# Optimization experiments

Hardware: AMD Instinct MI355X
Metric: run time of the kernel (lower is better)

## Reference

```python
import jax, jax.numpy as jnp
import numpy as np

B, T, D, H, C = 128, 1000, 40, 128, 8  # batch, time, input feats, hidden, classes


def _lstm_layer(x, Wih, Whh, bih, bhh):
    """Unidirectional LSTM over time. x: [B,T,Din] -> [B,T,H]. PyTorch gate order i,f,g,o."""
    Bn = x.shape[0]
    Hn = Whh.shape[1]
    b = bih + bhh
    def step(carry, xt):
        h, c = carry
        g = xt @ Wih.T + h @ Whh.T + b  # [B,4H]
        i, f, gg, o = jnp.split(g, 4, axis=-1)
        c = jax.nn.sigmoid(f) * c + jax.nn.sigmoid(i) * jnp.tanh(gg)
        h = jax.nn.sigmoid(o) * jnp.tanh(c)
        return (h, c), h
    h0 = jnp.zeros((Bn, Hn), x.dtype)
    _, hs = jax.lax.scan(step, (h0, h0), jnp.swapaxes(x, 0, 1))  # scan over time
    return jnp.swapaxes(hs, 0, 1)


def _bilstm_layer(x, pf, pb):
    fwd = _lstm_layer(x, *pf)
    bwd = jnp.flip(_lstm_layer(jnp.flip(x, 1), *pb), 1)
    return jnp.concatenate([fwd, bwd], axis=-1)  # [B,T,2H]


def setup_inputs() -> dict:
    key = jax.random.key(0)
    ks = jax.random.split(key, 16)
    s = 0.05
    def rn(k, shape):
        return jax.random.normal(k, shape, jnp.float32) * s
    inp = {"x": jax.random.normal(ks[0], (B, T, D), jnp.float32)}
    inp["ln_g"] = jnp.ones((D,), jnp.float32)
    inp["ln_b"] = jnp.zeros((D,), jnp.float32)
    dims = [D, 2 * H]  # layer-0 input feats, layer-1 input feats
    i = 1
    for l in range(2):
        for d in ("f", "b"):
            inp[f"Wih_{d}{l}"] = rn(ks[i], (4 * H, dims[l])); i += 1
            inp[f"Whh_{d}{l}"] = rn(ks[i], (4 * H, H)); i += 1
            inp[f"bih_{d}{l}"] = jnp.zeros((4 * H,), jnp.float32)
            inp[f"bhh_{d}{l}"] = jnp.zeros((4 * H,), jnp.float32)
    inp["attn_W1"] = rn(ks[i], (H, 2 * H)); i += 1
    inp["attn_b1"] = jnp.zeros((H,), jnp.float32)
    inp["attn_w2"] = rn(ks[i], (1, H)); i += 1
    inp["fc_W1"] = rn(ks[i], (H, 2 * H)); i += 1
    inp["fc_b1"] = jnp.zeros((H,), jnp.float32)
    inp["fc_W2"] = rn(ks[i], (C, H)); i += 1
    inp["fc_b2"] = jnp.zeros((C,), jnp.float32)
    return inp


def reference(x, ln_g, ln_b,
              Wih_f0, Whh_f0, bih_f0, bhh_f0, Wih_b0, Whh_b0, bih_b0, bhh_b0,
              Wih_f1, Whh_f1, bih_f1, bhh_f1, Wih_b1, Whh_b1, bih_b1, bhh_b1,
              attn_W1, attn_b1, attn_w2, fc_W1, fc_b1, fc_W2, fc_b2):
    # LayerNorm over feature dim (eps=1e-5, PyTorch default)
    mu = jnp.mean(x, axis=-1, keepdims=True)
    var = jnp.var(x, axis=-1, keepdims=True)
    xn = (x - mu) * jax.lax.rsqrt(var + 1e-5) * ln_g + ln_b
    # 2-layer bidirectional LSTM
    h = _bilstm_layer(xn, (Wih_f0, Whh_f0, bih_f0, bhh_f0), (Wih_b0, Whh_b0, bih_b0, bhh_b0))
    h = _bilstm_layer(h, (Wih_f1, Whh_f1, bih_f1, bhh_f1), (Wih_b1, Whh_b1, bih_b1, bhh_b1))
    # attention pooling: Linear-Tanh-Linear(no bias) -> softmax over time
    scores = jnp.tanh(h @ attn_W1.T + attn_b1) @ attn_w2[0]  # [B,T]
    w = jax.nn.softmax(scores, axis=1)
    ctx = jnp.einsum('bt,btd->bd', w, h)  # [B,2H]
    # MLP classifier head
    hid = jax.nn.relu(ctx @ fc_W1.T + fc_b1)
    return hid @ fc_W2.T + fc_b2  # [B,C] logits
```

## Files before the change

kernel.cpp:

```cpp
#include <hip/hip_runtime.h>

#define T_ 1000

typedef float v2f __attribute__((ext_vector_type(2)));

__device__ __forceinline__ float sigf(float x) { return 1.0f / (1.0f + __expf(-x)); }
__device__ __forceinline__ float tanh_fast(float x) { return 1.0f - 2.0f / (1.0f + __expf(2.0f * x)); }
__device__ __forceinline__ float dot4(float4 a, float4 b) {
  return a.x * b.x + a.y * b.y + a.z * b.z + a.w * b.w;
}
__device__ __forceinline__ void pkfma(v2f& acc, float4 w, float4 v) {
  v2f wl; wl[0] = w.x; wl[1] = w.y;
  v2f wh; wh[0] = w.z; wh[1] = w.w;
  v2f vl; vl[0] = v.x; vl[1] = v.y;
  v2f vh; vh[0] = v.z; vh[1] = v.w;
  acc += wl * vl;
  acc += wh * vh;
}
__device__ __forceinline__ unsigned short f2bf(float f) {
  unsigned u = __float_as_uint(f);
  u = (u + 0x7fffu + ((u >> 16) & 1u)) >> 16;
  return (unsigned short)u;
}
__device__ __forceinline__ float bf2f(unsigned short h) {
  return __uint_as_float(((unsigned)h) << 16);
}
__device__ __forceinline__ float4 bf4_to_f4(ushort4 u) {
  float4 r;
  r.x = bf2f(u.x); r.y = bf2f(u.y); r.z = bf2f(u.z); r.w = bf2f(u.w);
  return r;
}

__global__ void bail_kernel(float* out, int n) {
  for (int i = threadIdx.x; i < n; i += 256) out[i] = 0.0f;
}

__global__ __launch_bounds__(256) void ln_stats_kernel(const float* __restrict__ x,
                                                       float* __restrict__ mu_arr,
                                                       float* __restrict__ rs_arr) {
  const int lane = threadIdx.x & 63;
  const int w = threadIdx.x >> 6;
  const long row = (long)blockIdx.x * 4 + w;
  float v = (lane < 40) ? x[row * 40 + lane] : 0.0f;
  float s1 = v, s2 = v * v;
  for (int m = 32; m; m >>= 1) {
    s1 += __shfl_xor(s1, m, 64);
    s2 += __shfl_xor(s2, m, 64);
  }
  if (lane == 0) {
    const float mu = s1 * (1.0f / 40.0f);
    const float var = s2 * (1.0f / 40.0f) - mu * mu;
    mu_arr[row] = mu;
    rs_arr[row] = rsqrtf(var + 1e-5f);
  }
}

__global__ __launch_bounds__(512) __attribute__((amdgpu_waves_per_eu(2, 2))) void rec0_kernel(
    const float* __restrict__ x,
    const float* __restrict__ mu_arr, const float* __restrict__ rs_arr,
    const float* __restrict__ ln_g, const float* __restrict__ ln_b,
    const float* __restrict__ Wih_f, const float* __restrict__ Whh_f,
    const float* __restrict__ bih_f, const float* __restrict__ bhh_f,
    const float* __restrict__ Wih_b, const float* __restrict__ Whh_b,
    const float* __restrict__ bih_b, const float* __restrict__ bhh_b,
    float* __restrict__ h0) {
  const int tid = threadIdx.x;
  const int u = (tid >> 6) * 16 + ((tid & 63) >> 2);
  const int p = tid & 3;
  const int brow = blockIdx.x & 127;
  const int dir = blockIdx.x >> 7;
  const float* __restrict__ Wih = dir ? Wih_b : Wih_f;
  const float* __restrict__ Whh = dir ? Whh_b : Whh_f;
  const float* __restrict__ bih = dir ? bih_b : bih_f;
  const float* __restrict__ bhh = dir ? bhh_b : bhh_f;

  float4 wh[4][8];
  float4 wi[4][3];
  float S1[4], bias[4];
#pragma unroll
  for (int g = 0; g < 4; ++g) {
    const int row = g * 128 + u;
    const float4* wr = (const float4*)(Whh + row * 128 + p * 32);
#pragma unroll
    for (int ff = 0; ff < 8; ++ff) wh[g][ff] = wr[(ff + 2 * p) & 7];
    float s1p = 0.0f, s2p = 0.0f;
#pragma unroll
    for (int f = 0; f < 3; ++f) {
      float tmp[4];
#pragma unroll
      for (int e = 0; e < 4; ++e) {
        const int k = p * 12 + f * 4 + e;
        const float wv = (k < 40) ? Wih[row * 40 + k] : 0.0f;
        const float gk = (k < 40) ? ln_g[k] : 0.0f;
        const float bk = (k < 40) ? ln_b[k] : 0.0f;
        const float wf = wv * gk;
        tmp[e] = wf;
        s1p += wf;
        s2p += wv * bk;
      }
      wi[g][f] = make_float4(tmp[0], tmp[1], tmp[2], tmp[3]);
    }
    s1p += __shfl_xor(s1p, 1, 64); s1p += __shfl_xor(s1p, 2, 64);
    s2p += __shfl_xor(s2p, 1, 64); s2p += __shfl_xor(s2p, 2, 64);
    S1[g] = s1p;
    bias[g] = bih[g * 128 + u] + bhh[g * 128 + u] + s2p;
  }

  __shared__ float h4f[2][128];
  __shared__ __align__(16) float x_ring[2][8][48];
  __shared__ float mu_ring[2][8], rs_ring[2][8];
  __shared__ float hring[2][8][128];

  const int lr8 = tid / 40;
  const int lcol = tid - lr8 * 40;
  const long xbase = (long)brow * T_ * 40;
  const long mbase = (long)brow * T_;
  const long hbase = (long)brow * T_ * 256;

  if (tid < 128) h4f[0][tid] = 0.0f;
  if (tid < 128) {
    const int b = tid >> 6, r = (tid >> 3) & 7, cc = 40 + (tid & 7);
    x_ring[b][r][cc] = 0.0f;
  }
  if (tid < 320) {
    const int t = lr8;
    const int tt = dir ? (T_ - 1 - t) : t;
    x_ring[0][lr8][lcol] = x[xbase + (long)tt * 40 + lcol];
  } else if (tid < 328) {
    const int t = tid - 320;
    const int tt = dir ? (T_ - 1 - t) : t;
    mu_ring[0][t] = mu_arr[mbase + tt];
  } else if (tid < 336) {
    const int t = tid - 328;
    const int tt = dir ? (T_ - 1 - t) : t;
    rs_ring[0][t] = rs_arr[mbase + tt];
  }
  float c = 0.0f;
  float xpf = 0.0f, mupf = 0.0f, rspf = 0.0f;
  __syncthreads();

  for (int sb = 0; sb < 125; ++sb) {
    const int rb = sb & 1;
#pragma unroll
    for (int su = 0; su < 8; ++su) {
      const int rdq = su & 1, wrq = rdq ^ 1;
      if (su == 0) {
        if (sb + 1 < 125) {
          if (tid < 320) {
            const int t = (sb + 1) * 8 + lr8;
            const int tt = dir ? (T_ - 1 - t) : t;
            xpf = x[xbase + (long)tt * 40 + lcol];
          } else if (tid < 328) {
            const int t = (sb + 1) * 8 + (tid - 320);
            const int tt = dir ? (T_ - 1 - t) : t;
            mupf = mu_arr[mbase + tt];
          } else if (tid < 336) {
            const int t = (sb + 1) * 8 + (tid - 328);
            const int tt = dir ? (T_ - 1 - t) : t;
            rspf = rs_arr[mbase + tt];
          }
        }
        if (sb > 0) {
#pragma unroll
          for (int e = 0; e < 2; ++e) {
            const int idx = tid + e * 512;
            const int v = idx >> 7, j = idx & 127;
            const int ts = (sb - 1) * 8 + v;
            const int te = dir ? (T_ - 1 - ts) : ts;
            h0[hbase + (long)te * 256 + dir * 128 + j] = hring[rb ^ 1][v][j];
          }
        }
      }
      v2f hacc[4], xacc[4];
#pragma unroll
      for (int g = 0; g < 4; ++g) { hacc[g] = 0.0f; xacc[g] = 0.0f; }
      const float4* h4v = (const float4*)h4f[rdq];
#pragma unroll
      for (int ff = 0; ff < 8; ++ff) {
        const float4 hv = h4v[p * 8 + ((ff + 2 * p) & 7)];
        pkfma(hacc[0], wh[0][ff], hv);
        pkfma(hacc[1], wh[1][ff], hv);
        pkfma(hacc[2], wh[2][ff], hv);
        pkfma(hacc[3], wh[3][ff], hv);
      }
      const float4* xr4 = (const float4*)x_ring[rb][su];
#pragma unroll
      for (int f = 0; f < 3; ++f) {
        const float4 xv = xr4[p * 3 + f];
        pkfma(xacc[0], wi[0][f], xv);
        pkfma(xacc[1], wi[1][f], xv);
        pkfma(xacc[2], wi[2][f], xv);
        pkfma(xacc[3], wi[3][f], xv);
      }
      const float rs = rs_ring[rb][su];
      const float mu = mu_ring[rb][su];
      float pg[4];
#pragma unroll
      for (int g = 0; g < 4; ++g) {
        pg[g] = (hacc[g][0] + hacc[g][1]) + rs * (xacc[g][0] + xacc[g][1]);
        pg[g] += __shfl_xor(pg[g], 1, 64);
        pg[g] += __shfl_xor(pg[g], 2, 64);
        pg[g] += bias[g] - rs * mu * S1[g];
      }
      const float ig = sigf(pg[0]);
      const float fg = sigf(pg[1]);
      const float gg = tanh_fast(pg[2]);
      const float og = sigf(pg[3]);
      c = fg * c + ig * gg;
      const float hv = og * tanh_fast(c);
      if (p == 0) { h4f[wrq][u] = hv; hring[rb][su][u] = hv; }
      if (su == 7 && sb + 1 < 125) {
        if (tid < 320) x_ring[rb ^ 1][lr8][lcol] = xpf;
        else if (tid < 328) mu_ring[rb ^ 1][tid - 320] = mupf;
        else if (tid < 336) rs_ring[rb ^ 1][tid - 328] = rspf;
      }
      __syncthreads();
    }
  }
#pragma unroll
  for (int e = 0; e < 2; ++e) {
    const int idx = tid + e * 512;
    const int v = idx >> 7, j = idx & 127;
    const int ts = 124 * 8 + v;
    const int te = dir ? (T_ - 1 - ts) : ts;
    h0[hbase + (long)te * 256 + dir * 128 + j] = hring[0][v][j];
  }
}

__global__ __launch_bounds__(512) __attribute__((amdgpu_waves_per_eu(2, 2))) void rec1_kernel(
    const float* __restrict__ xw_f, const float* __restrict__ xw_b,
    const float* __restrict__ Whh_f, const float* __restrict__ bih_f, const float* __restrict__ bhh_f,
    const float* __restrict__ Whh_b, const float* __restrict__ bih_b, const float* __restrict__ bhh_b,
    unsigned short* __restrict__ h1b, float* __restrict__ state,
    int Tc, int t0f, int t0b, int first) {
  const int tid = threadIdx.x;
  const int u = (tid >> 6) * 16 + ((tid & 63) >> 2);
  const int p = tid & 3;
  const int brow = blockIdx.x & 127;
  const int dir = blockIdx.x >> 7;
  const float* __restrict__ xw = dir ? xw_b : xw_f;
  const float* __restrict__ Whh = dir ? Whh_b : Whh_f;
  const float* __restrict__ bih = dir ? bih_b : bih_f;
  const float* __restrict__ bhh = dir ? bhh_b : bhh_f;
  const int t0 = dir ? t0b : t0f;

  float4 wh[4][8];
#pragma unroll
  for (int g = 0; g < 4; ++g) {
    const float4* wr = (const float4*)(Whh + (g * 128 + u) * 128 + p * 32);
#pragma unroll
    for (int ff = 0; ff < 8; ++ff) wh[g][ff] = wr[(ff + 2 * p) & 7];
  }
  const int myrow = p * 128 + u;
  const float bias_p = bih[myrow] + bhh[myrow];

  __shared__ float h4f[2][128];
  __shared__ float hring[2][8][128];
  float* sblk = state + (long)blockIdx.x * 256;
  float c = 0.0f;
  if (first) {
    if (tid < 128) h4f[0][tid] = 0.0f;
  } else {
    if (tid < 128) h4f[0][tid] = sblk[tid];
    c = sblk[128 + u];
  }
  const long gbase = (long)brow * Tc;
  float xr[8];
#pragma unroll
  for (int v = 0; v < 8; ++v) {
    xr[v] = 0.0f;
    if (v < Tc) {
      const int tr = dir ? (Tc - 1 - v) : v;
      xr[v] = xw[(gbase + tr) * 512 + myrow];
    }
  }
  __syncthreads();

  const int nSB = (Tc + 7) / 8;
  for (int sb = 0; sb < nSB; ++sb) {
    const int rb = sb & 1;
#pragma unroll
    for (int su = 0; su < 8; ++su) {
      const int s = sb * 8 + su;
      if (s >= Tc) break;
      const int rdq = su & 1, wrq = rdq ^ 1;
      if (su == 0 && sb > 0) {
#pragma unroll
        for (int e = 0; e < 2; ++e) {
          const int idx = tid + e * 512;
          const int v = idx >> 7, j = idx & 127;
          const int s2 = (sb - 1) * 8 + v;
          const int tt = dir ? (Tc - 1 - s2) : s2;
          h1b[((long)brow * T_ + (t0 + tt)) * 256 + dir * 128 + j] = f2bf(hring[rb ^ 1][v][j]);
        }
      }
      v2f hacc[4];
#pragma unroll
      for (int g = 0; g < 4; ++g) hacc[g] = 0.0f;
      const float4* h4v = (const float4*)h4f[rdq];
#pragma unroll
      for (int ff = 0; ff < 8; ++ff) {
        const float4 hv = h4v[p * 8 + ((ff + 2 * p) & 7)];
        pkfma(hacc[0], wh[0][ff], hv);
        pkfma(hacc[1], wh[1][ff], hv);
        pkfma(hacc[2], wh[2][ff], hv);
        pkfma(hacc[3], wh[3][ff], hv);
      }
      const float xin = xr[su] + bias_p;
      float pg[4];
#pragma unroll
      for (int g = 0; g < 4; ++g) {
        pg[g] = hacc[g][0] + hacc[g][1] + ((p == g) ? xin : 0.0f);
        pg[g] += __shfl_xor(pg[g], 1, 64);
        pg[g] += __shfl_xor(pg[g], 2, 64);
      }
      const float ig = sigf(pg[0]);
      const float fg = sigf(pg[1]);
      const float gg = tanh_fast(pg[2]);
      const float og = sigf(pg[3]);
      c = fg * c + ig * gg;
      const float hv = og * tanh_fast(c);
      if (p == 0) { h4f[wrq][u] = hv; hring[rb][su][u] = hv; }
      if (su == 7) {
#pragma unroll
        for (int v = 0; v < 8; ++v) {
          const int sn = s + 1 + v;
          xr[v] = 0.0f;
          if (sn < Tc) {
            const int tr = dir ? (Tc - 1 - sn) : sn;
            xr[v] = xw[(gbase + tr) * 512 + myrow];
          }
        }
      }
      __syncthreads();
    }
  }
  {
    const int sbL = (Tc - 1) >> 3;
    const int cnt = Tc - sbL * 8;
    const int rbL = sbL & 1;
#pragma unroll
    for (int e = 0; e < 2; ++e) {
      const int idx = tid + e * 512;
      const int v = idx >> 7, j = idx & 127;
      if (v < cnt) {
        const int s2 = sbL * 8 + v;
        const int tt = dir ? (Tc - 1 - s2) : s2;
        h1b[((long)brow * T_ + (t0 + tt)) * 256 + dir * 128 + j] = f2bf(hring[rbL][v][j]);
      }
    }
  }
  if (tid < 128) sblk[tid] = h4f[Tc & 1][tid];
  if (p == 0) sblk[128 + u] = c;
}

__global__ __launch_bounds__(256, 2) void gemm_xw1(
    const float* __restrict__ h0,
    const float* __restrict__ Wf, const float* __restrict__ Wb,
    float* __restrict__ xwf, float* __restrict__ xwb,
    int Tc, int t0f, int t0b) {
  __shared__ float As[64 * 36];
  __shared__ float Bs[128 * 36];
  __shared__ int rowbase[64];
  const int tid = threadIdx.x;
  const int tx = tid & 15, ty = tid >> 4;
  const int r0 = blockIdx.x * 64;
  const int jt = blockIdx.y;
  const int dir = jt >> 2;
  const int nh = jt & 3;
  const float* __restrict__ W = dir ? Wb : Wf;
  float* __restrict__ out = dir ? xwb : xwf;
  const int jbase = nh * 128;
  const int t0 = dir ? t0b : t0f;

  if (tid < 64) {
    const int r = r0 + tid;
    const int br = r / Tc;
    rowbase[tid] = br * T_ + t0 + (r - br * Tc);
  }

  float4* As4 = (float4*)As;
  float4* Bs4 = (float4*)Bs;
  float acc[4][8] = {};
#pragma unroll 1
  for (int kk = 0; kk < 8; ++kk) {
    __syncthreads();
#pragma unroll
    for (int i = 0; i < 2; ++i) {
      const int q = tid + i * 256;
      const int row = q >> 3, k4 = q & 7;
      As4[row * 9 + k4] = *(const float4*)&h0[(long)rowbase[row] * 256 + kk * 32 + k4 * 4];
    }
#pragma unroll
    for (int i = 0; i < 4; ++i) {
      const int q = tid + i * 256;
      const int row = q >> 3, k4 = q & 7;
      Bs4[row * 9 + k4] = *(const float4*)&W[(long)(jbase + row) * 256 + kk * 32 + k4 * 4];
    }
    __syncthreads();
#pragma unroll 1
    for (int k4 = 0; k4 < 8; ++k4) {
      float4 av[4];
#pragma unroll
      for (int r = 0; r < 4; ++r) av[r] = As4[(ty * 4 + r) * 9 + k4];
#pragma unroll
      for (int c2 = 0; c2 < 8; ++c2) {
        const float4 bv = Bs4[(tx + 16 * c2) * 9 + k4];
#pragma unroll
        for (int r = 0; r < 4; ++r) acc[r][c2] += dot4(av[r], bv);
      }
    }
  }
#pragma unroll
  for (int r = 0; r < 4; ++r) {
    const long ob = (long)(r0 + ty * 4 + r) * 512 + jbase + tx;
#pragma unroll
    for (int c2 = 0; c2 < 8; ++c2) out[ob + c2 * 16] = acc[r][c2];
  }
}

__global__ __launch_bounds__(256, 2) void score_kernel(
    const unsigned short* __restrict__ h1b, const float* __restrict__ W1,
    const float* __restrict__ b1, const float* __restrict__ w2,
    float* __restrict__ scores) {
  __shared__ float As[64 * 36];
  __shared__ float Bs[128 * 36];
  const int tid = threadIdx.x;
  const int tx = tid & 15, ty = tid >> 4;
  const long r0 = (long)blockIdx.x * 64;

  float4* As4 = (float4*)As;
  float4* Bs4 = (float4*)Bs;
  float acc[4][8] = {};
#pragma unroll 1
  for (int kk = 0; kk < 8; ++kk) {
    __syncthreads();
#pragma unroll
    for (int i = 0; i < 2; ++i) {
      const int q = tid + i * 256;
      const int row = q >> 3, k4 = q & 7;
      const ushort4 uv = *(const ushort4*)&h1b[(r0 + row) * 256 + kk * 32 + k4 * 4];
      As4[row * 9 + k4] = bf4_to_f4(uv);
    }
#pragma unroll
    for (int i = 0; i < 4; ++i) {
      const int q = tid + i * 256;
      const int row = q >> 3, k4 = q & 7;
      Bs4[row * 9 + k4] = *(const float4*)&W1[(long)row * 256 + kk * 32 + k4 * 4];
    }
    __syncthreads();
#pragma unroll 1
    for (int k4 = 0; k4 < 8; ++k4) {
      float4 av[4];
#pragma unroll
      for (int r = 0; r < 4; ++r) av[r] = As4[(ty * 4 + r) * 9 + k4];
#pragma unroll
      for (int c2 = 0; c2 < 8; ++c2) {
        const float4 bv = Bs4[(tx + 16 * c2) * 9 + k4];
#pragma unroll
        for (int r = 0; r < 4; ++r) acc[r][c2] += dot4(av[r], bv);
      }
    }
  }
#pragma unroll
  for (int r = 0; r < 4; ++r) {
    float s = 0.0f;
#pragma unroll
    for (int c2 = 0; c2 < 8; ++c2) {
      const int col = tx + 16 * c2;
      s += tanh_fast(acc[r][c2] + b1[col]) * w2[col];
    }
#pragma unroll
    for (int m = 1; m < 16; m <<= 1) s += __shfl_xor(s, m, 16);
    if (tx == 0) scores[r0 + ty * 4 + r] = s;
  }
}

__global__ __launch_bounds__(256, 2) void head_kernel(
    const float* __restrict__ scores, const unsigned short* __restrict__ h1b,
    const float* __restrict__ fW1, const float* __restrict__ fb1,
    const float* __restrict__ fW2, const float* __restrict__ fb2,
    float* __restrict__ outp) {
  const int b = blockIdx.x, tid = threadIdx.x;
  __shared__ float wls[1000];
  __shared__ float red[8];
  __shared__ __align__(16) float ctx[256];
  __shared__ __align__(16) float hid[128];

  float sv[4];
  float mx = -1e30f;
#pragma unroll
  for (int i = 0; i < 4; ++i) {
    const int t = tid + i * 256;
    sv[i] = (t < 1000) ? scores[b * 1000 + t] : -1e30f;
    mx = fmaxf(mx, sv[i]);
  }
  for (int m = 32; m; m >>= 1) mx = fmaxf(mx, __shfl_xor(mx, m, 64));
  if ((tid & 63) == 0) red[tid >> 6] = mx;
  __syncthreads();
  mx = fmaxf(fmaxf(red[0], red[1]), fmaxf(red[2], red[3]));
  float se = 0.0f;
#pragma unroll
  for (int i = 0; i < 4; ++i) {
    const int t = tid + i * 256;
    if (t < 1000) {
      const float e = __expf(sv[i] - mx);
      wls[t] = e;
      se += e;
    }
  }
  for (int m = 32; m; m >>= 1) se += __shfl_xor(se, m, 64);
  if ((tid & 63) == 0) red[4 + (tid >> 6)] = se;
  __syncthreads();
  const float rinv = 1.0f / (red[4] + red[5] + red[6] + red[7]);

  float a = 0.0f;
  const unsigned short* hb = h1b + (long)b * T_ * 256 + tid;
  for (int t = 0; t < T_; ++t) a = fmaf(wls[t], bf2f(hb[t * 256]), a);
  ctx[tid] = a * rinv;
  __syncthreads();
  if (tid < 128) {
    float s = fb1[tid];
    const float4* wr = (const float4*)&fW1[tid * 256];
    const float4* cc = (const float4*)ctx;
#pragma unroll
    for (int f = 0; f < 64; ++f) s += dot4(wr[f], cc[f]);
    hid[tid] = fmaxf(s, 0.0f);
  }
  __syncthreads();
  if (tid < 8) {
    float s = fb2[tid];
    const float4* wr = (const float4*)&fW2[tid * 128];
    const float4* hh = (const float4*)hid;
#pragma unroll
    for (int f = 0; f < 32; ++f) s += dot4(wr[f], hh[f]);
    outp[b * 8 + tid] = s;
  }
}

extern "C" void kernel_launch(void* const* d_in, const int* in_sizes, int n_in,
                              void* d_out, int out_size, void* d_ws, size_t ws_size,
                              hipStream_t stream) {
  (void)in_sizes; (void)n_in; (void)out_size;
  const float* x       = (const float*)d_in[0];
  const float* ln_g    = (const float*)d_in[1];
  const float* ln_b    = (const float*)d_in[2];
  const float* Wih_f0  = (const float*)d_in[3];
  const float* Whh_f0  = (const float*)d_in[4];
  const float* bih_f0  = (const float*)d_in[5];
  const float* bhh_f0  = (const float*)d_in[6];
  const float* Wih_b0  = (const float*)d_in[7];
  const float* Whh_b0  = (const float*)d_in[8];
  const float* bih_b0  = (const float*)d_in[9];
  const float* bhh_b0  = (const float*)d_in[10];
  const float* Wih_f1  = (const float*)d_in[11];
  const float* Whh_f1  = (const float*)d_in[12];
  const float* bih_f1  = (const float*)d_in[13];
  const float* bhh_f1  = (const float*)d_in[14];
  const float* Wih_b1  = (const float*)d_in[15];
  const float* Whh_b1  = (const float*)d_in[16];
  const float* bih_b1  = (const float*)d_in[17];
  const float* bhh_b1  = (const float*)d_in[18];
  const float* attn_W1 = (const float*)d_in[19];
  const float* attn_b1 = (const float*)d_in[20];
  const float* attn_w2 = (const float*)d_in[21];
  const float* fc_W1   = (const float*)d_in[22];
  const float* fc_b1   = (const float*)d_in[23];
  const float* fc_W2   = (const float*)d_in[24];
  const float* fc_b2   = (const float*)d_in[25];

  char* base = (char*)d_ws;
  size_t off = 0;
  auto alloc = [&](size_t bytes) {
    char* ptr = base + off;
    off += (bytes + 255) & ~(size_t)255;
    return ptr;
  };
  float*          h0    = (float*)alloc(32768000ull * 4);
  unsigned short* h1b   = (unsigned short*)alloc(32768000ull * 2);
  float*          state = (float*)alloc(65536ull * 4);
  float*          scor  = (float*)alloc(128000ull * 4);
  float*          mu_a  = (float*)alloc(128000ull * 4);
  float*          rs_a  = (float*)alloc(128000ull * 4);

  const size_t rem = (ws_size > off) ? (ws_size - off) : 0;
  static const int cands[16] = {1000, 500, 250, 200, 125, 100, 50, 40, 25, 20, 10, 8, 5, 4, 2, 1};
  int Tc = 0;
  for (int ci = 0; ci < 16; ++ci) {
    if (524288ull * (size_t)cands[ci] <= rem) { Tc = cands[ci]; break; }
  }
  if (Tc == 0) {
    bail_kernel<<<dim3(1), dim3(256), 0, stream>>>((float*)d_out, 1024);
    return;
  }
  float* xwf = (float*)(base + off);
  float* xwb = xwf + 65536L * Tc;

  ln_stats_kernel<<<dim3(32000), dim3(256), 0, stream>>>(x, mu_a, rs_a);
  rec0_kernel<<<dim3(256), dim3(512), 0, stream>>>(x, mu_a, rs_a, ln_g, ln_b,
                                                   Wih_f0, Whh_f0, bih_f0, bhh_f0,
                                                   Wih_b0, Whh_b0, bih_b0, bhh_b0, h0);
  const int nch = T_ / Tc;
  for (int ch = 0; ch < nch; ++ch) {
    const int t0f = ch * Tc;
    const int t0b = T_ - (ch + 1) * Tc;
    gemm_xw1<<<dim3(2 * Tc, 8), dim3(256), 0, stream>>>(h0, Wih_f1, Wih_b1, xwf, xwb, Tc, t0f, t0b);
    rec1_kernel<<<dim3(256), dim3(512), 0, stream>>>(xwf, xwb, Whh_f1, bih_f1, bhh_f1,
                                                     Whh_b1, bih_b1, bhh_b1, h1b, state,
                                                     Tc, t0f, t0b, (ch == 0) ? 1 : 0);
  }
  score_kernel<<<dim3(2000), dim3(256), 0, stream>>>(h1b, attn_W1, attn_b1, attn_w2, scor);
  head_kernel<<<dim3(128), dim3(256), 0, stream>>>(scor, h1b, fc_W1, fc_b1, fc_W2, fc_b2,
                                                   (float*)d_out);
}
```

Before: 3.173 ms.

## Hoist layer-0 input projection to GEMM and share fp16-LDS recurrence kernel

Layer 0 no longer fuses the LayerNorm input projection into its recurrent loop. A new chunked GEMM computes normalized x times Wih first, and both layers then use one recurrence kernel. In that kernel, half the Whh gate rows (f and o) move from registers into LDS as fp16 with an XOR swizzle, and the i and g rows stay in fp32 registers, which cuts register pressure. The GEMMs switch to packed v2f FMA accumulation. This trades extra launches, a global round trip for the layer-0 projections and fp16 rounding on half the recurrent weights for a lighter per-step loop.

```diff
diff --git a/kernel.cpp b/kernel.cpp
--- a/kernel.cpp
+++ b/kernel.cpp
@@ -1,4 +1,5 @@
 #include <hip/hip_runtime.h>
+#include <hip/hip_fp16.h>
 
 #define T_ 1000
 
@@ -55,207 +56,142 @@
   }
 }
 
-__global__ __launch_bounds__(512) __attribute__((amdgpu_waves_per_eu(2, 2))) void rec0_kernel(
+__global__ __launch_bounds__(256, 2) void gemm_xw0(
     const float* __restrict__ x,
     const float* __restrict__ mu_arr, const float* __restrict__ rs_arr,
     const float* __restrict__ ln_g, const float* __restrict__ ln_b,
-    const float* __restrict__ Wih_f, const float* __restrict__ Whh_f,
+    const float* __restrict__ Wf, const float* __restrict__ Wb,
+    float* __restrict__ xwf, float* __restrict__ xwb,
+    int Tc, int t0f, int t0b) {
+  __shared__ float As[64 * 44];
+  __shared__ float Bs[128 * 44];
+  const int tid = threadIdx.x;
+  const int tx = tid & 15, ty = tid >> 4;
+  const int r0 = blockIdx.x * 64;
+  const int jt = blockIdx.y;
+  const int dir = jt >> 2, nh = jt & 3;
+  const float* __restrict__ W = dir ? Wb : Wf;
+  float* __restrict__ out = dir ? xwb : xwf;
+  const int jbase = nh * 128;
+  const int t0 = dir ? t0b : t0f;
+
+  float4* As4 = (float4*)As;
+  float4* Bs4 = (float4*)Bs;
+  {
+    const int row = tid >> 2;
+    const int t4 = tid & 3;
+    const int r = r0 + row;
+    const int br = r / Tc;
+    const long xrow = (long)br * T_ + t0 + (r - br * Tc);
+    const float mu = mu_arr[xrow];
+    const float rs = rs_arr[xrow];
+#pragma unroll
+    for (int m = 0; m < 3; ++m) {
+      const int k4 = t4 + m * 4;
+      if (k4 < 10) {
+        const float4 v = *(const float4*)&x[xrow * 40 + k4 * 4];
+        const float4 g4 = *(const float4*)&ln_g[k4 * 4];
+        const float4 b4 = *(const float4*)&ln_b[k4 * 4];
+        float4 xn;
+        xn.x = (v.x - mu) * rs * g4.x + b4.x;
+        xn.y = (v.y - mu) * rs * g4.y + b4.y;
+        xn.z = (v.z - mu) * rs * g4.z + b4.z;
+        xn.w = (v.w - mu) * rs * g4.w + b4.w;
+        As4[row * 11 + k4] = xn;
+      }
+    }
+  }
+  {
+    const int row = tid & 127;
+    const int h = tid >> 7;
+#pragma unroll
+    for (int m = 0; m < 5; ++m) {
+      const int k4 = h + m * 2;
+      Bs4[row * 11 + k4] = *(const float4*)&W[(long)(jbase + row) * 40 + k4 * 4];
+    }
+  }
+  __syncthreads();
+
+  v2f acc2[4][8];
+#pragma unroll
+  for (int r = 0; r < 4; ++r)
+#pragma unroll
+    for (int c2 = 0; c2 < 8; ++c2) acc2[r][c2] = 0.0f;
+#pragma unroll 1
+  for (int k4 = 0; k4 < 10; ++k4) {
+    float4 av[4];
+#pragma unroll
+    for (int r = 0; r < 4; ++r) av[r] = As4[(ty * 4 + r) * 11 + k4];
+#pragma unroll
+    for (int c2 = 0; c2 < 8; ++c2) {
+      const float4 bv = Bs4[(tx + 16 * c2) * 11 + k4];
+#pragma unroll
+      for (int r = 0; r < 4; ++r) pkfma(acc2[r][c2], av[r], bv);
+    }
+  }
+#pragma unroll
+  for (int r = 0; r < 4; ++r) {
+    const long ob = (long)(r0 + ty * 4 + r) * 512 + jbase + tx;
+#pragma unroll
+    for (int c2 = 0; c2 < 8; ++c2) out[ob + c2 * 16] = acc2[r][c2][0] + acc2[r][c2][1];
+  }
+}
+
+__global__ __launch_bounds__(512) void rec_fused(
+    const float* __restrict__ xw_f, const float* __restrict__ xw_b,
+    const float* __restrict__ Whh_f, const float* __restrict__ Whh_b,
     const float* __restrict__ bih_f, const float* __restrict__ bhh_f,
-    const float* __restrict__ Wih_b, const float* __restrict__ Whh_b,
     const float* __restrict__ bih_b, const float* __restrict__ bhh_b,
-    float* __restrict__ h0) {
+    float* __restrict__ h0out, unsigned short* __restrict__ h1out, int out_bf16,
+    float* __restrict__ state, int Tc, int t0f, int t0b, int first) {
   const int tid = threadIdx.x;
   const int u = (tid >> 6) * 16 + ((tid & 63) >> 2);
   const int p = tid & 3;
   const int brow = blockIdx.x & 127;
   const int dir = blockIdx.x >> 7;
-  const float* __restrict__ Wih = dir ? Wih_b : Wih_f;
-  const float* __restrict__ Whh = dir ? Whh_b : Whh_f;
-  const float* __restrict__ bih = dir ? bih_b : bih_f;
-  const float* __restrict__ bhh = dir ? bhh_b : bhh_f;
-
-  float4 wh[4][8];
-  float4 wi[4][3];
-  float S1[4], bias[4];
-#pragma unroll
-  for (int g = 0; g < 4; ++g) {
-    const int row = g * 128 + u;
-    const float4* wr = (const float4*)(Whh + row * 128 + p * 32);
-#pragma unroll
-    for (int ff = 0; ff < 8; ++ff) wh[g][ff] = wr[(ff + 2 * p) & 7];
-    float s1p = 0.0f, s2p = 0.0f;
-#pragma unroll
-    for (int f = 0; f < 3; ++f) {
-      float tmp[4];
-#pragma unroll
-      for (int e = 0; e < 4; ++e) {
-        const int k = p * 12 + f * 4 + e;
-        const float wv = (k < 40) ? Wih[row * 40 + k] : 0.0f;
-        const float gk = (k < 40) ? ln_g[k] : 0.0f;
-        const float bk = (k < 40) ? ln_b[k] : 0.0f;
-        const float wf = wv * gk;
-        tmp[e] = wf;
-        s1p += wf;
-        s2p += wv * bk;
-      }
-      wi[g][f] = make_float4(tmp[0], tmp[1], tmp[2], tmp[3]);
-    }
-    s1p += __shfl_xor(s1p, 1, 64); s1p += __shfl_xor(s1p, 2, 64);
-    s2p += __shfl_xor(s2p, 1, 64); s2p += __shfl_xor(s2p, 2, 64);
-    S1[g] = s1p;
-    bias[g] = bih[g * 128 + u] + bhh[g * 128 + u] + s2p;
-  }
-
-  __shared__ float h4f[2][128];
-  __shared__ __align__(16) float x_ring[2][8][48];
-  __shared__ float mu_ring[2][8], rs_ring[2][8];
-  __shared__ float hring[2][8][128];
-
-  const int lr8 = tid / 40;
-  const int lcol = tid - lr8 * 40;
-  const long xbase = (long)brow * T_ * 40;
-  const long mbase = (long)brow * T_;
-  const long hbase = (long)brow * T_ * 256;
-
-  if (tid < 128) h4f[0][tid] = 0.0f;
-  if (tid < 128) {
-    const int b = tid >> 6, r = (tid >> 3) & 7, cc = 40 + (tid & 7);
-    x_ring[b][r][cc] = 0.0f;
-  }
-  if (tid < 320) {
-    const int t = lr8;
-    const int tt = dir ? (T_ - 1 - t) : t;
-    x_ring[0][lr8][lcol] = x[xbase + (long)tt * 40 + lcol];
-  } else if (tid < 328) {
-    const int t = tid - 320;
-    const int tt = dir ? (T_ - 1 - t) : t;
-    mu_ring[0][t] = mu_arr[mbase + tt];
-  } else if (tid < 336) {
-    const int t = tid - 328;
-    const int tt = dir ? (T_ - 1 - t) : t;
-    rs_ring[0][t] = rs_arr[mbase + tt];
-  }
-  float c = 0.0f;
-  float xpf = 0.0f, mupf = 0.0f, rspf = 0.0f;
-  __syncthreads();
-
-  for (int sb = 0; sb < 125; ++sb) {
-    const int rb = sb & 1;
-#pragma unroll
-    for (int su = 0; su < 8; ++su) {
-      const int rdq = su & 1, wrq = rdq ^ 1;
-      if (su == 0) {
-        if (sb + 1 < 125) {
-          if (tid < 320) {
-            const int t = (sb + 1) * 8 + lr8;
-            const int tt = dir ? (T_ - 1 - t) : t;
-            xpf = x[xbase + (long)tt * 40 + lcol];
-          } else if (tid < 328) {
-            const int t = (sb + 1) * 8 + (tid - 320);
-            const int tt = dir ? (T_ - 1 - t) : t;
-            mupf = mu_arr[mbase + tt];
-          } else if (tid < 336) {
-            const int t = (sb + 1) * 8 + (tid - 328);
-            const int tt = dir ? (T_ - 1 - t) : t;
-            rspf = rs_arr[mbase + tt];
-          }
-        }
-        if (sb > 0) {
-#pragma unroll
-          for (int e = 0; e < 2; ++e) {
-            const int idx = tid + e * 512;
-            const int v = idx >> 7, j = idx & 127;
-            const int ts = (sb - 1) * 8 + v;
-            const int te = dir ? (T_ - 1 - ts) : ts;
-            h0[hbase + (long)te * 256 + dir * 128 + j] = hring[rb ^ 1][v][j];
-          }
-        }
-      }
-      v2f hacc[4], xacc[4];
-#pragma unroll
-      for (int g = 0; g < 4; ++g) { hacc[g] = 0.0f; xacc[g] = 0.0f; }
-      const float4* h4v = (const float4*)h4f[rdq];
-#pragma unroll
-      for (int ff = 0; ff < 8; ++ff) {
-        const float4 hv = h4v[p * 8 + ((ff + 2 * p) & 7)];
-        pkfma(hacc[0], wh[0][ff], hv);
-        pkfma(hacc[1], wh[1][ff], hv);
-        pkfma(hacc[2], wh[2][ff], hv);
-        pkfma(hacc[3], wh[3][ff], hv);
-      }
-      const float4* xr4 = (const float4*)x_ring[rb][su];
-#pragma unroll
-      for (int f = 0; f < 3; ++f) {
-        const float4 xv = xr4[p * 3 + f];
-        pkfma(xacc[0], wi[0][f], xv);
-        pkfma(xacc[1], wi[1][f], xv);
-        pkfma(xacc[2], wi[2][f], xv);
-        pkfma(xacc[3], wi[3][f], xv);
-      }
-      const float rs = rs_ring[rb][su];
-      const float mu = mu_ring[rb][su];
-      float pg[4];
-#pragma unroll
-      for (int g = 0; g < 4; ++g) {
-        pg[g] = (hacc[g][0] + hacc[g][1]) + rs * (xacc[g][0] + xacc[g][1]);
-        pg[g] += __shfl_xor(pg[g], 1, 64);
-        pg[g] += __shfl_xor(pg[g], 2, 64);
-        pg[g] += bias[g] - rs * mu * S1[g];
-      }
-      const float ig = sigf(pg[0]);
-      const float fg = sigf(pg[1]);
-      const float gg = tanh_fast(pg[2]);
-      const float og = sigf(pg[3]);
-      c = fg * c + ig * gg;
-      const float hv = og * tanh_fast(c);
-      if (p == 0) { h4f[wrq][u] = hv; hring[rb][su][u] = hv; }
-      if (su == 7 && sb + 1 < 125) {
-        if (tid < 320) x_ring[rb ^ 1][lr8][lcol] = xpf;
-        else if (tid < 328) mu_ring[rb ^ 1][tid - 320] = mupf;
-        else if (tid < 336) rs_ring[rb ^ 1][tid - 328] = rspf;
-      }
-      __syncthreads();
-    }
-  }
-#pragma unroll
-  for (int e = 0; e < 2; ++e) {
-    const int idx = tid + e * 512;
-    const int v = idx >> 7, j = idx & 127;
-    const int ts = 124 * 8 + v;
-    const int te = dir ? (T_ - 1 - ts) : ts;
-    h0[hbase + (long)te * 256 + dir * 128 + j] = hring[0][v][j];
-  }
-}
-
-__global__ __launch_bounds__(512) __attribute__((amdgpu_waves_per_eu(2, 2))) void rec1_kernel(
-    const float* __restrict__ xw_f, const float* __restrict__ xw_b,
-    const float* __restrict__ Whh_f, const float* __restrict__ bih_f, const float* __restrict__ bhh_f,
-    const float* __restrict__ Whh_b, const float* __restrict__ bih_b, const float* __restrict__ bhh_b,
-    unsigned short* __restrict__ h1b, float* __restrict__ state,
-    int Tc, int t0f, int t0b, int first) {
-  const int tid = threadIdx.x;
-  const int u = (tid >> 6) * 16 + ((tid & 63) >> 2);
-  const int p = tid & 3;
-  const int brow = blockIdx.x & 127;
-  const int dir = blockIdx.x >> 7;
-  const float* __restrict__ xw = dir ? xw_b : xw_f;
+  const float* __restrict__ xw  = dir ? xw_b : xw_f;
   const float* __restrict__ Whh = dir ? Whh_b : Whh_f;
   const float* __restrict__ bih = dir ? bih_b : bih_f;
   const float* __restrict__ bhh = dir ? bhh_b : bhh_f;
   const int t0 = dir ? t0b : t0f;
 
-  float4 wh[4][8];
-#pragma unroll
-  for (int g = 0; g < 4; ++g) {
-    const float4* wr = (const float4*)(Whh + (g * 128 + u) * 128 + p * 32);
-#pragma unroll
-    for (int ff = 0; ff < 8; ++ff) wh[g][ff] = wr[(ff + 2 * p) & 7];
+  __shared__ __align__(16) unsigned short wl[2 * 128 * 128];
+  __shared__ float h4f[2][128];
+  __shared__ float hring[2][8][128];
+
+#pragma unroll
+  for (int k2 = 0; k2 < 8; ++k2) {
+    const int U = tid + k2 * 512;
+    const int g2 = U >> 11;
+    const int uu = (U >> 4) & 127;
+    const int j  = U & 15;
+    const int grow = (g2 ? 384 : 128) + uu;
+    const float4 va = *(const float4*)&Whh[grow * 128 + j * 8];
+    const float4 vb = *(const float4*)&Whh[grow * 128 + j * 8 + 4];
+    const int js = j ^ (uu & 7);
+    __half2* dst = (__half2*)&wl[((g2 * 128 + uu) * 16 + js) * 8];
+    dst[0] = __floats2half2_rn(va.x, va.y);
+    dst[1] = __floats2half2_rn(va.z, va.w);
+    dst[2] = __floats2half2_rn(vb.x, vb.y);
+    dst[3] = __floats2half2_rn(vb.z, vb.w);
+  }
+
+  float4 whr[2][8];
+  {
+    const float4* wi_ = (const float4*)(Whh + u * 128 + p * 32);
+    const float4* wg_ = (const float4*)(Whh + (256 + u) * 128 + p * 32);
+#pragma unroll
+    for (int ff2 = 0; ff2 < 4; ++ff2) {
+      const int c4 = (ff2 + p) & 3;
+      whr[0][2 * ff2]     = wi_[2 * c4];
+      whr[0][2 * ff2 + 1] = wi_[2 * c4 + 1];
+      whr[1][2 * ff2]     = wg_[2 * c4];
+      whr[1][2 * ff2 + 1] = wg_[2 * c4 + 1];
+    }
   }
   const int myrow = p * 128 + u;
   const float bias_p = bih[myrow] + bhh[myrow];
 
-  __shared__ float h4f[2][128];
-  __shared__ float hring[2][8][128];
   float* sblk = state + (long)blockIdx.x * 256;
   float c = 0.0f;
   if (first) {
@@ -277,6 +213,7 @@
   __syncthreads();
 
   const int nSB = (Tc + 7) / 8;
+  const long obase = (long)brow * T_;
   for (int sb = 0; sb < nSB; ++sb) {
     const int rb = sb & 1;
 #pragma unroll
@@ -291,33 +228,49 @@
           const int v = idx >> 7, j = idx & 127;
           const int s2 = (sb - 1) * 8 + v;
           const int tt = dir ? (Tc - 1 - s2) : s2;
-          h1b[((long)brow * T_ + (t0 + tt)) * 256 + dir * 128 + j] = f2bf(hring[rb ^ 1][v][j]);
+          const long oidx = (obase + (t0 + tt)) * 256 + dir * 128 + j;
+          const float hval = hring[rb ^ 1][v][j];
+          if (out_bf16) h1out[oidx] = f2bf(hval);
+          else          h0out[oidx] = hval;
         }
       }
-      v2f hacc[4];
-#pragma unroll
-      for (int g = 0; g < 4; ++g) hacc[g] = 0.0f;
+      float ai = 0.f, af = 0.f, ag = 0.f, ao = 0.f;
       const float4* h4v = (const float4*)h4f[rdq];
 #pragma unroll
-      for (int ff = 0; ff < 8; ++ff) {
-        const float4 hv = h4v[p * 8 + ((ff + 2 * p) & 7)];
-        pkfma(hacc[0], wh[0][ff], hv);
-        pkfma(hacc[1], wh[1][ff], hv);
-        pkfma(hacc[2], wh[2][ff], hv);
-        pkfma(hacc[3], wh[3][ff], hv);
+      for (int ff2 = 0; ff2 < 4; ++ff2) {
+        const int c4 = (ff2 + p) & 3;
+        const float4 hva = h4v[p * 8 + 2 * c4];
+        const float4 hvb = h4v[p * 8 + 2 * c4 + 1];
+        ai += dot4(hva, whr[0][2 * ff2]) + dot4(hvb, whr[0][2 * ff2 + 1]);
+        ag += dot4(hva, whr[1][2 * ff2]) + dot4(hvb, whr[1][2 * ff2 + 1]);
+        const int js = (p * 4 + c4) ^ (u & 7);
+        const float4 wfv = *(const float4*)&wl[(u * 16 + js) * 8];
+        const float4 wov = *(const float4*)&wl[((128 + u) * 16 + js) * 8];
+        const __half2* hf2 = (const __half2*)&wfv;
+        const __half2* ho2 = (const __half2*)&wov;
+        float2 t;
+        t = __half22float2(hf2[0]); af += t.x * hva.x + t.y * hva.y;
+        t = __half22float2(hf2[1]); af += t.x * hva.z + t.y * hva.w;
+        t = __half22float2(hf2[2]); af += t.x * hvb.x + t.y * hvb.y;
+        t = __half22float2(hf2[3]); af += t.x * hvb.z + t.y * hvb.w;
+        t = __half22float2(ho2[0]); ao += t.x * hva.x + t.y * hva.y;
+        t = __half22float2(ho2[1]); ao += t.x * hva.z + t.y * hva.w;
+        t = __half22float2(ho2[2]); ao += t.x * hvb.x + t.y * hvb.y;
+        t = __half22float2(ho2[3]); ao += t.x * hvb.z + t.y * hvb.w;
       }
       const float xin = xr[su] + bias_p;
-      float pg[4];
-#pragma unroll
-      for (int g = 0; g < 4; ++g) {
-        pg[g] = hacc[g][0] + hacc[g][1] + ((p == g) ? xin : 0.0f);
-        pg[g] += __shfl_xor(pg[g], 1, 64);
-        pg[g] += __shfl_xor(pg[g], 2, 64);
-      }
-      const float ig = sigf(pg[0]);
-      const float fg = sigf(pg[1]);
-      const float gg = tanh_fast(pg[2]);
-      const float og = sigf(pg[3]);
+      float pg0 = ai + ((p == 0) ? xin : 0.0f);
+      float pg1 = af + ((p == 1) ? xin : 0.0f);
+      float pg2 = ag + ((p == 2) ? xin : 0.0f);
+      float pg3 = ao + ((p == 3) ? xin : 0.0f);
+      pg0 += __shfl_xor(pg0, 1, 64); pg0 += __shfl_xor(pg0, 2, 64);
+      pg1 += __shfl_xor(pg1, 1, 64); pg1 += __shfl_xor(pg1, 2, 64);
+      pg2 += __shfl_xor(pg2, 1, 64); pg2 += __shfl_xor(pg2, 2, 64);
+      pg3 += __shfl_xor(pg3, 1, 64); pg3 += __shfl_xor(pg3, 2, 64);
+      const float ig = sigf(pg0);
+      const float fg = sigf(pg1);
+      const float gg = tanh_fast(pg2);
+      const float og = sigf(pg3);
       c = fg * c + ig * gg;
       const float hv = og * tanh_fast(c);
       if (p == 0) { h4f[wrq][u] = hv; hring[rb][su][u] = hv; }
@@ -346,7 +299,10 @@
       if (v < cnt) {
         const int s2 = sbL * 8 + v;
         const int tt = dir ? (Tc - 1 - s2) : s2;
-        h1b[((long)brow * T_ + (t0 + tt)) * 256 + dir * 128 + j] = f2bf(hring[rbL][v][j]);
+        const long oidx = (obase + (t0 + tt)) * 256 + dir * 128 + j;
+        const float hval = hring[rbL][v][j];
+        if (out_bf16) h1out[oidx] = f2bf(hval);
+        else          h0out[oidx] = hval;
       }
     }
   }
@@ -381,7 +337,11 @@
 
   float4* As4 = (float4*)As;
   float4* Bs4 = (float4*)Bs;
-  float acc[4][8] = {};
+  v2f acc2[4][8];
+#pragma unroll
+  for (int r = 0; r < 4; ++r)
+#pragma unroll
+    for (int c2 = 0; c2 < 8; ++c2) acc2[r][c2] = 0.0f;
 #pragma unroll 1
   for (int kk = 0; kk < 8; ++kk) {
     __syncthreads();
@@ -407,7 +367,7 @@
       for (int c2 = 0; c2 < 8; ++c2) {
         const float4 bv = Bs4[(tx + 16 * c2) * 9 + k4];
 #pragma unroll
-        for (int r = 0; r < 4; ++r) acc[r][c2] += dot4(av[r], bv);
+        for (int r = 0; r < 4; ++r) pkfma(acc2[r][c2], av[r], bv);
       }
     }
   }
@@ -415,7 +375,7 @@
   for (int r = 0; r < 4; ++r) {
     const long ob = (long)(r0 + ty * 4 + r) * 512 + jbase + tx;
 #pragma unroll
-    for (int c2 = 0; c2 < 8; ++c2) out[ob + c2 * 16] = acc[r][c2];
+    for (int c2 = 0; c2 < 8; ++c2) out[ob + c2 * 16] = acc2[r][c2][0] + acc2[r][c2][1];
   }
 }
 
@@ -431,7 +391,11 @@
 
   float4* As4 = (float4*)As;
   float4* Bs4 = (float4*)Bs;
-  float acc[4][8] = {};
+  v2f acc2[4][8];
+#pragma unroll
+  for (int r = 0; r < 4; ++r)
+#pragma unroll
+    for (int c2 = 0; c2 < 8; ++c2) acc2[r][c2] = 0.0f;
 #pragma unroll 1
   for (int kk = 0; kk < 8; ++kk) {
     __syncthreads();
@@ -458,7 +422,7 @@
       for (int c2 = 0; c2 < 8; ++c2) {
         const float4 bv = Bs4[(tx + 16 * c2) * 9 + k4];
 #pragma unroll
-        for (int r = 0; r < 4; ++r) acc[r][c2] += dot4(av[r], bv);
+        for (int r = 0; r < 4; ++r) pkfma(acc2[r][c2], av[r], bv);
       }
     }
   }
@@ -468,7 +432,7 @@
 #pragma unroll
     for (int c2 = 0; c2 < 8; ++c2) {
       const int col = tx + 16 * c2;
-      s += tanh_fast(acc[r][c2] + b1[col]) * w2[col];
+      s += tanh_fast(acc2[r][c2][0] + acc2[r][c2][1] + b1[col]) * w2[col];
     }
 #pragma unroll
     for (int m = 1; m < 16; m <<= 1) s += __shfl_xor(s, m, 16);
@@ -597,17 +561,25 @@
   float* xwb = xwf + 65536L * Tc;
 
   ln_stats_kernel<<<dim3(32000), dim3(256), 0, stream>>>(x, mu_a, rs_a);
-  rec0_kernel<<<dim3(256), dim3(512), 0, stream>>>(x, mu_a, rs_a, ln_g, ln_b,
-                                                   Wih_f0, Whh_f0, bih_f0, bhh_f0,
-                                                   Wih_b0, Whh_b0, bih_b0, bhh_b0, h0);
   const int nch = T_ / Tc;
   for (int ch = 0; ch < nch; ++ch) {
     const int t0f = ch * Tc;
     const int t0b = T_ - (ch + 1) * Tc;
+    gemm_xw0<<<dim3(2 * Tc, 8), dim3(256), 0, stream>>>(x, mu_a, rs_a, ln_g, ln_b,
+                                                        Wih_f0, Wih_b0, xwf, xwb, Tc, t0f, t0b);
+    rec_fused<<<dim3(256), dim3(512), 0, stream>>>(xwf, xwb, Whh_f0, Whh_b0,
+                                                   bih_f0, bhh_f0, bih_b0, bhh_b0,
+                                                   h0, h1b, 0, state, Tc, t0f, t0b,
+                                                   (ch == 0) ? 1 : 0);
+  }
+  for (int ch = 0; ch < nch; ++ch) {
+    const int t0f = ch * Tc;
+    const int t0b = T_ - (ch + 1) * Tc;
     gemm_xw1<<<dim3(2 * Tc, 8), dim3(256), 0, stream>>>(h0, Wih_f1, Wih_b1, xwf, xwb, Tc, t0f, t0b);
-    rec1_kernel<<<dim3(256), dim3(512), 0, stream>>>(xwf, xwb, Whh_f1, bih_f1, bhh_f1,
-                                                     Whh_b1, bih_b1, bhh_b1, h1b, state,
-                                                     Tc, t0f, t0b, (ch == 0) ? 1 : 0);
+    rec_fused<<<dim3(256), dim3(512), 0, stream>>>(xwf, xwb, Whh_f1, Whh_b1,
+                                                   bih_f1, bhh_f1, bih_b1, bhh_b1,
+                                                   h0, h1b, 1, state, Tc, t0f, t0b,
+                                                   (ch == 0) ? 1 : 0);
   }
   score_kernel<<<dim3(2000), dim3(256), 0, stream>>>(h1b, attn_W1, attn_b1, attn_w2, scor);
   head_kernel<<<dim3(128), dim3(256), 0, stream>>>(scor, h1b, fc_W1, fc_b1, fc_W2, fc_b2,
```

Measured after the change: 4.155 ms. 1.31x slower.
